# Kernel tuning notes

Hardware: AMD Instinct MI355X
Metric: run time of the kernel (lower is better)

The kernel has to match this reference:

```python
import jax, jax.numpy as jnp
import numpy as np

N_NODES = 100000


def gcn_conv(x, src, dst, W, b):
    # torch_geometric GCNConv: add self-loops, sym-normalize, linear, aggregate
    n = x.shape[0]
    deg = jax.ops.segment_sum(jnp.ones_like(src, dtype=x.dtype), dst, num_segments=n)
    dinv = jnp.where(deg > 0, jax.lax.rsqrt(deg), 0.0)
    norm = dinv[src] * dinv[dst]                      # [E]
    h = x @ W                                         # [N, out]
    msg = h[src] * norm[:, None]                      # [E, out] gather
    out = jax.ops.segment_sum(msg, dst, num_segments=n)  # scatter-add
    return out + b


def add_self_loops(edge_index, n):
    loop = jnp.arange(n, dtype=edge_index.dtype)
    src = jnp.concatenate([edge_index[0], loop])
    dst = jnp.concatenate([edge_index[1], loop])
    return src, dst


def setup_inputs() -> dict:
    key = jax.random.key(0)
    k1, k2, k3, k4 = jax.random.split(key, 4)
    F_in, F_mid = 64, 32
    x = jax.random.normal(k1, (N_NODES, F_in), dtype=jnp.float32)
    edge_index = jax.random.randint(k2, (2, 1200000), 0, N_NODES, dtype=jnp.int64)
    W1 = jax.random.normal(k3, (F_in, F_mid), dtype=jnp.float32) * (1.0 / np.sqrt(F_in))
    b1 = jnp.zeros((F_mid,), dtype=jnp.float32)
    W2 = jax.random.normal(k4, (F_mid, F_in), dtype=jnp.float32) * (1.0 / np.sqrt(F_mid))
    b2 = jnp.zeros((F_in,), dtype=jnp.float32)
    return {"x": x, "edge_index": edge_index, "W1": W1, "b1": b1, "W2": W2, "b2": b2}


def reference(x, edge_index, W1, b1, W2, b2):
    src, dst = add_self_loops(edge_index, x.shape[0])
    h = jax.nn.relu(gcn_conv(x, src, dst, W1, b1))
    # F.dropout in eval mode is identity (module not in training)
    out = gcn_conv(h, src, dst, W2, b2)
    return out
```

## Files before the change

kernel.cpp:

```cpp
#include <hip/hip_runtime.h>


#define CAP 32
#define OVF_MAX 65536
#define SH_BITS 8
#define SH 256
#define BCAP 3584
#define EPB 4096
#define EPT 16

__device__ __forceinline__ unsigned bf16rn(float f) {
    unsigned u = __float_as_uint(f);
    return (u + 0x7fffu + ((u >> 16) & 1u)) >> 16;
}
__device__ __forceinline__ unsigned pack2(float f0, float f1) {
    return (bf16rn(f1) << 16) | bf16rn(f0);
}
__device__ __forceinline__ void acc2(float4& a, uint2 v) {
    a.x += __uint_as_float(v.x << 16);
    a.y += __uint_as_float(v.x & 0xffff0000u);
    a.z += __uint_as_float(v.y << 16);
    a.w += __uint_as_float(v.y & 0xffff0000u);
}

__global__ void init_kernel(int* __restrict__ bcur, int* __restrict__ ovfcnt,
                            unsigned int* __restrict__ g1rowN,
                            unsigned int* __restrict__ q1rowN, int B) {
    int i = blockIdx.x * blockDim.x + threadIdx.x;
    if (i < B) bcur[i] = i * BCAP;
    if (i == 0) *ovfcnt = 0;
    if (i < 16) { g1rowN[i] = 0u; q1rowN[i] = 0u; }
}

__global__ __launch_bounds__(256) void bin_kernel(const int* __restrict__ src,
                                                  const int* __restrict__ dst,
                                                  int* __restrict__ bcur,
                                                  unsigned int* __restrict__ ebuf,
                                                  int* __restrict__ ovfcnt,
                                                  int* __restrict__ ovf, int E, int B) {
    __shared__ int h[512];
    __shared__ int gp[512];
    for (int b = threadIdx.x; b < B; b += 256) h[b] = 0;
    __syncthreads();
    int base = blockIdx.x * EPB;
    int s[EPT], d[EPT], r[EPT];
#pragma unroll
    for (int k = 0; k < EPT; ++k) {
        int e = base + k * 256 + threadIdx.x;
        bool ok = e < E;
        s[k] = ok ? src[e] : 0;
        d[k] = ok ? dst[e] : 0;
        r[k] = ok ? atomicAdd(&h[d[k] >> SH_BITS], 1) : 0;
    }
    __syncthreads();
    for (int b = threadIdx.x; b < B; b += 256)
        if (h[b]) gp[b] = atomicAdd(&bcur[b], h[b]);
    __syncthreads();
#pragma unroll
    for (int k = 0; k < EPT; ++k) {
        int e = base + k * 256 + threadIdx.x;
        if (e < E) {
            int bk = d[k] >> SH_BITS;
            int pos = gp[bk] + r[k];
            if (pos < (bk + 1) * BCAP)
                ebuf[pos] = ((unsigned)(d[k] & (SH - 1)) << 24) | (unsigned)s[k];
            else { int o = atomicAdd(ovfcnt, 1); if (o < OVF_MAX) { ovf[2 * o] = s[k]; ovf[2 * o + 1] = d[k]; } }
        }
    }
}

__global__ __launch_bounds__(256) void fillb_kernel(const unsigned int* __restrict__ ebuf,
                                                    const int* __restrict__ bcur,
                                                    int* __restrict__ adj,
                                                    float* __restrict__ dinv,
                                                    int* __restrict__ ovfcnt,
                                                    int* __restrict__ ovf, int N) {
    __shared__ int lcnt[SH];
    __shared__ int ladj[SH * CAP];
    int b = blockIdx.x;
    for (int i = threadIdx.x; i < SH; i += 256) lcnt[i] = 0;
    for (int i = threadIdx.x; i < SH * CAP; i += 256) ladj[i] = N;
    __syncthreads();
    int beg = b * BCAP;
    int tot = bcur[b] - beg;
    int m = tot < BCAP ? tot : BCAP;
    for (int i = threadIdx.x; i < m; i += 256) {
        unsigned p = ebuf[beg + i];
        int ld = (int)(p >> 24), sidx = (int)(p & 0xFFFFFF);
        int q = atomicAdd(&lcnt[ld], 1);
        if (q < CAP) ladj[ld * CAP + q] = sidx;
        else { int o = atomicAdd(ovfcnt, 1); if (o < OVF_MAX) { ovf[2 * o] = sidx; ovf[2 * o + 1] = (b << SH_BITS) + ld; } }
    }
    __syncthreads();
    int nb0 = b << SH_BITS;
    const int4* l4 = (const int4*)ladj;
    int4* a4 = (int4*)(adj + (size_t)nb0 * CAP);
    for (int i = threadIdx.x; i < SH * CAP / 4; i += 256) {
        int row = i >> 3;
        int nd = nb0 + row;
        bool second = (i & 4) != 0;
        if (nd < N && (!second || lcnt[row] >= 16)) a4[i] = l4[i];
    }
    for (int i = threadIdx.x; i < SH; i += 256) {
        int nd = nb0 + i;
        if (nd < N) dinv[nd] = rsqrtf((float)lcnt[i] + 1.0f);
    }
}

__global__ __launch_bounds__(256) void gemm1_kernel(const float* __restrict__ x,
                                                    const float* __restrict__ W1,
                                                    const float* __restrict__ dinv,
                                                    unsigned int* __restrict__ g1, int N) {
    __shared__ float Ws[64 * 32];
    __shared__ float xs[16][64];
    int tid = threadIdx.x;
    const float4* W4 = (const float4*)W1;
    float4* Ws4 = (float4*)Ws;
    for (int i = tid; i < 512; i += 256) Ws4[i] = W4[i];
    int nb = blockIdx.x * 16;
    {
        int ln = tid >> 4, k4 = (tid & 15) * 4;
        int n = nb + ln;
        float4 v = make_float4(0.f, 0.f, 0.f, 0.f);
        if (n < N) v = *(const float4*)(x + (size_t)n * 64 + k4);
        *(float4*)(&xs[ln][k4]) = v;
    }
    __syncthreads();
    int ln = tid >> 4, j = tid & 15;
    int n = nb + ln;
    if (n < N) {
        float s0 = 0.f, s1 = 0.f;
#pragma unroll
        for (int k = 0; k < 64; ++k) {
            float xv = xs[ln][k];
            s0 += xv * Ws[k * 32 + 2 * j];
            s1 += xv * Ws[k * 32 + 2 * j + 1];
        }
        float dv = dinv[n];
        g1[(size_t)n * 16 + j] = pack2(dv * s0, dv * s1);
    }
}

__device__ __forceinline__ float4 gather_row4(const int2* __restrict__ adj2,
                                              const int* __restrict__ ovfcnt,
                                              const int* __restrict__ ovf,
                                              const uint2* __restrict__ g2,
                                              int n, int l, int N) {
    int2 h1 = adj2[(size_t)n * 16 + l];
    float4 a = make_float4(0.f, 0.f, 0.f, 0.f);
    uint2 self = g2[(size_t)n * 8 + l];
    int s15;
    {
        int s0  = __shfl(h1.x, 0, 8), s1  = __shfl(h1.y, 0, 8);
        int s2  = __shfl(h1.x, 1, 8), s3  = __shfl(h1.y, 1, 8);
        int s4  = __shfl(h1.x, 2, 8), s5  = __shfl(h1.y, 2, 8);
        int s6  = __shfl(h1.x, 3, 8), s7  = __shfl(h1.y, 3, 8);
        int s8  = __shfl(h1.x, 4, 8), s9  = __shfl(h1.y, 4, 8);
        int s10 = __shfl(h1.x, 5, 8), s11 = __shfl(h1.y, 5, 8);
        int s12 = __shfl(h1.x, 6, 8), s13 = __shfl(h1.y, 6, 8);
        int s14 = __shfl(h1.x, 7, 8); s15 = __shfl(h1.y, 7, 8);
        uint2 v0  = g2[(size_t)s0  * 8 + l], v1  = g2[(size_t)s1  * 8 + l];
        uint2 v2  = g2[(size_t)s2  * 8 + l], v3  = g2[(size_t)s3  * 8 + l];
        uint2 v4  = g2[(size_t)s4  * 8 + l], v5  = g2[(size_t)s5  * 8 + l];
        uint2 v6  = g2[(size_t)s6  * 8 + l], v7  = g2[(size_t)s7  * 8 + l];
        uint2 v8  = g2[(size_t)s8  * 8 + l], v9  = g2[(size_t)s9  * 8 + l];
        uint2 v10 = g2[(size_t)s10 * 8 + l], v11 = g2[(size_t)s11 * 8 + l];
        uint2 v12 = g2[(size_t)s12 * 8 + l], v13 = g2[(size_t)s13 * 8 + l];
        uint2 v14 = g2[(size_t)s14 * 8 + l], v15 = g2[(size_t)s15 * 8 + l];
        acc2(a, self);
        acc2(a, v0);  acc2(a, v1);  acc2(a, v2);  acc2(a, v3);
        acc2(a, v4);  acc2(a, v5);  acc2(a, v6);  acc2(a, v7);
        acc2(a, v8);  acc2(a, v9);  acc2(a, v10); acc2(a, v11);
        acc2(a, v12); acc2(a, v13); acc2(a, v14); acc2(a, v15);
    }
    if (s15 != N) {
        int2 h2 = adj2[(size_t)n * 16 + 8 + l];
        int s0  = __shfl(h2.x, 0, 8), s1  = __shfl(h2.y, 0, 8);
        int s2  = __shfl(h2.x, 1, 8), s3  = __shfl(h2.y, 1, 8);
        int s4  = __shfl(h2.x, 2, 8), s5  = __shfl(h2.y, 2, 8);
        int s6  = __shfl(h2.x, 3, 8), s7  = __shfl(h2.y, 3, 8);
        int s8  = __shfl(h2.x, 4, 8), s9  = __shfl(h2.y, 4, 8);
        int s10 = __shfl(h2.x, 5, 8), s11 = __shfl(h2.y, 5, 8);
        int s12 = __shfl(h2.x, 6, 8), s13 = __shfl(h2.y, 6, 8);
        int s14 = __shfl(h2.x, 7, 8), sl15 = __shfl(h2.y, 7, 8);
        uint2 v0  = g2[(size_t)s0  * 8 + l], v1  = g2[(size_t)s1  * 8 + l];
        uint2 v2  = g2[(size_t)s2  * 8 + l], v3  = g2[(size_t)s3  * 8 + l];
        uint2 v4  = g2[(size_t)s4  * 8 + l], v5  = g2[(size_t)s5  * 8 + l];
        uint2 v6  = g2[(size_t)s6  * 8 + l], v7  = g2[(size_t)s7  * 8 + l];
        uint2 v8  = g2[(size_t)s8  * 8 + l], v9  = g2[(size_t)s9  * 8 + l];
        uint2 v10 = g2[(size_t)s10 * 8 + l], v11 = g2[(size_t)s11 * 8 + l];
        uint2 v12 = g2[(size_t)s12 * 8 + l], v13 = g2[(size_t)s13 * 8 + l];
        uint2 v14 = g2[(size_t)s14 * 8 + l], v15 = g2[(size_t)sl15 * 8 + l];
        acc2(a, v0);  acc2(a, v1);  acc2(a, v2);  acc2(a, v3);
        acc2(a, v4);  acc2(a, v5);  acc2(a, v6);  acc2(a, v7);
        acc2(a, v8);  acc2(a, v9);  acc2(a, v10); acc2(a, v11);
        acc2(a, v12); acc2(a, v13); acc2(a, v14); acc2(a, v15);
    }
    int c = *ovfcnt; if (c > OVF_MAX) c = OVF_MAX;
    for (int i = 0; i < c; ++i) {
        if (ovf[2 * i + 1] == n) acc2(a, g2[(size_t)ovf[2 * i] * 8 + l]);
    }
    return a;
}

__global__ void gather_q_kernel(const int2* __restrict__ adj2,
                                const int* __restrict__ ovfcnt, const int* __restrict__ ovf,
                                const uint2* __restrict__ g2, const float* __restrict__ dinv,
                                const float* __restrict__ b1, uint2* __restrict__ q2, int N) {
    int tid = blockIdx.x * blockDim.x + threadIdx.x;
    int n = tid >> 3, l = tid & 7;
    if (n < N) {
        float4 a = gather_row4(adj2, ovfcnt, ovf, g2, n, l, N);
        float dv = dinv[n];
        float4 bb = ((const float4*)b1)[l];
        float vx = dv * a.x + bb.x, vy = dv * a.y + bb.y;
        float vz = dv * a.z + bb.z, vw = dv * a.w + bb.w;
        vx = vx > 0.f ? vx : 0.f; vy = vy > 0.f ? vy : 0.f;
        vz = vz > 0.f ? vz : 0.f; vw = vw > 0.f ? vw : 0.f;
        q2[(size_t)n * 8 + l] = make_uint2(pack2(dv * vx, dv * vy), pack2(dv * vz, dv * vw));
    }
}

__global__ __launch_bounds__(256) void gather_out_kernel(
        const int2* __restrict__ adj2,
        const int* __restrict__ ovfcnt, const int* __restrict__ ovf,
        const uint2* __restrict__ q2, const float* __restrict__ dinv,
        const float* __restrict__ W2, const float* __restrict__ b2,
        float* __restrict__ out, int N) {
    __shared__ float Ws[32 * 64];
    __shared__ float sAgg[32][36];
    int tid = threadIdx.x;
    const float4* W4 = (const float4*)W2;
    float4* Ws4 = (float4*)Ws;
    for (int i = tid; i < 512; i += 256) Ws4[i] = W4[i];
    int nb = blockIdx.x * 32;
    int o = tid >> 3, l = tid & 7;
    int n = nb + o;
    if (n < N) *(float4*)(&sAgg[o][l * 4]) = gather_row4(adj2, ovfcnt, ovf, q2, n, l, N);
    __syncthreads();
    int ln = tid >> 6, j = tid & 63;
#pragma unroll
    for (int nn = 0; nn < 8; ++nn) {
        int ol = nn * 4 + ln;
        int node = nb + ol;
        if (node < N) {
            float s = 0.f;
#pragma unroll
            for (int k = 0; k < 32; ++k) s += sAgg[ol][k] * Ws[k * 64 + j];
            __builtin_nontemporal_store(dinv[node] * s + b2[j], &out[(size_t)node * 64 + j]);
        }
    }
}

extern "C" void kernel_launch(void* const* d_in, const int* in_sizes, int n_in,
                              void* d_out, int out_size, void* d_ws, size_t ws_size,
                              hipStream_t stream) {
    const float* x  = (const float*)d_in[0];
    const int*   ei = (const int*)d_in[1];
    const float* W1 = (const float*)d_in[2];
    const float* b1 = (const float*)d_in[3];
    const float* W2 = (const float*)d_in[4];
    const float* b2 = (const float*)d_in[5];
    float* out = (float*)d_out;

    int N = in_sizes[0] / 64;
    int E = in_sizes[1] / 2;
    const int* src = ei;
    const int* dst = ei + (size_t)E;
    int B = (N + SH - 1) >> SH_BITS;

    size_t NP = (size_t)N + 1;
    float* dinv   = (float*)d_ws;
    unsigned int* g1 = (unsigned int*)(dinv + N);
    unsigned int* q1 = g1 + 16 * NP;
    unsigned int* ebuf = q1;
    int*   adj    = (int*)(q1 + 16 * NP);
    int*   bcur   = adj + (size_t)CAP * N;
    int*   ovfcnt = bcur + 512;
    int*   ovf    = ovfcnt + 4;

    init_kernel<<<(B + 255) / 256, 256, 0, stream>>>(bcur, ovfcnt,
                                                     g1 + 16 * (size_t)N, q1 + 16 * (size_t)N, B);
    bin_kernel<<<(E + EPB - 1) / EPB, 256, 0, stream>>>(src, dst, bcur, ebuf, ovfcnt, ovf, E, B);
    fillb_kernel<<<B, 256, 0, stream>>>(ebuf, bcur, adj, dinv, ovfcnt, ovf, N);

    gemm1_kernel<<<(N + 15) / 16, 256, 0, stream>>>(x, W1, dinv, g1, N);

    long long tq = (long long)N * 8;
    gather_q_kernel<<<(int)((tq + 255) / 256), 256, 0, stream>>>(
        (const int2*)adj, ovfcnt, ovf, (const uint2*)g1, dinv, b1, (uint2*)q1, N);
    gather_out_kernel<<<(N + 31) / 32, 256, 0, stream>>>(
        (const int2*)adj, ovfcnt, ovf, (const uint2*)q1, dinv, W2, b2, out, N);
}
```

Measured before the change: 179.9 us.

## Split bf16 feature tables into column halves to shrink gather working set

The 32-wide bf16 intermediate tables g1 and q1 are split into two 16-column halves (ga/gb, qa/qb), each with 32-byte rows. The first-layer gather now runs as two passes over separate half tables, and the output gather walks the halves one after another. The aim is to make each pass's random-gather working set half as large so it fits better in cache. Nontemporal loads are also added for streamed inputs, and ebuf gets its own region instead of aliasing q1. In exchange, adjacency indices are read twice and each gathered access moves 4 bytes instead of 8, so more load instructions are issued.

```diff
diff --git a/kernel.cpp b/kernel.cpp
--- a/kernel.cpp
+++ b/kernel.cpp
@@ -9,6 +9,8 @@
 #define EPB 4096
 #define EPT 16
 
+typedef __attribute__((ext_vector_type(4))) float vf4;
+
 __device__ __forceinline__ unsigned bf16rn(float f) {
     unsigned u = __float_as_uint(f);
     return (u + 0x7fffu + ((u >> 16) & 1u)) >> 16;
@@ -16,20 +18,18 @@
 __device__ __forceinline__ unsigned pack2(float f0, float f1) {
     return (bf16rn(f1) << 16) | bf16rn(f0);
 }
-__device__ __forceinline__ void acc2(float4& a, uint2 v) {
-    a.x += __uint_as_float(v.x << 16);
-    a.y += __uint_as_float(v.x & 0xffff0000u);
-    a.z += __uint_as_float(v.y << 16);
-    a.w += __uint_as_float(v.y & 0xffff0000u);
+__device__ __forceinline__ void accu(float2& a, unsigned v) {
+    a.x += __uint_as_float(v << 16);
+    a.y += __uint_as_float(v & 0xffff0000u);
 }
 
 __global__ void init_kernel(int* __restrict__ bcur, int* __restrict__ ovfcnt,
-                            unsigned int* __restrict__ g1rowN,
-                            unsigned int* __restrict__ q1rowN, int B) {
+                            unsigned* __restrict__ ga, unsigned* __restrict__ gb,
+                            unsigned* __restrict__ qa, unsigned* __restrict__ qb, int B) {
     int i = blockIdx.x * blockDim.x + threadIdx.x;
     if (i < B) bcur[i] = i * BCAP;
     if (i == 0) *ovfcnt = 0;
-    if (i < 16) { g1rowN[i] = 0u; q1rowN[i] = 0u; }
+    if (i < 8) { ga[i] = 0u; gb[i] = 0u; qa[i] = 0u; qb[i] = 0u; }
 }
 
 __global__ __launch_bounds__(256) void bin_kernel(const int* __restrict__ src,
@@ -48,8 +48,8 @@
     for (int k = 0; k < EPT; ++k) {
         int e = base + k * 256 + threadIdx.x;
         bool ok = e < E;
-        s[k] = ok ? src[e] : 0;
-        d[k] = ok ? dst[e] : 0;
+        s[k] = ok ? __builtin_nontemporal_load(src + e) : 0;
+        d[k] = ok ? __builtin_nontemporal_load(dst + e) : 0;
         r[k] = ok ? atomicAdd(&h[d[k] >> SH_BITS], 1) : 0;
     }
     __syncthreads();
@@ -85,7 +85,7 @@
     int tot = bcur[b] - beg;
     int m = tot < BCAP ? tot : BCAP;
     for (int i = threadIdx.x; i < m; i += 256) {
-        unsigned p = ebuf[beg + i];
+        unsigned p = __builtin_nontemporal_load(ebuf + beg + i);
         int ld = (int)(p >> 24), sidx = (int)(p & 0xFFFFFF);
         int q = atomicAdd(&lcnt[ld], 1);
         if (q < CAP) ladj[ld * CAP + q] = sidx;
@@ -110,20 +110,21 @@
 __global__ __launch_bounds__(256) void gemm1_kernel(const float* __restrict__ x,
                                                     const float* __restrict__ W1,
                                                     const float* __restrict__ dinv,
-                                                    unsigned int* __restrict__ g1, int N) {
+                                                    unsigned int* __restrict__ ga,
+                                                    unsigned int* __restrict__ gb, int N) {
     __shared__ float Ws[64 * 32];
     __shared__ float xs[16][64];
     int tid = threadIdx.x;
-    const float4* W4 = (const float4*)W1;
-    float4* Ws4 = (float4*)Ws;
+    const vf4* W4 = (const vf4*)W1;
+    vf4* Ws4 = (vf4*)Ws;
     for (int i = tid; i < 512; i += 256) Ws4[i] = W4[i];
     int nb = blockIdx.x * 16;
     {
-        int ln = tid >> 4, k4 = (tid & 15) * 4;
+        int ln = tid >> 4, k4 = tid & 15;
         int n = nb + ln;
-        float4 v = make_float4(0.f, 0.f, 0.f, 0.f);
-        if (n < N) v = *(const float4*)(x + (size_t)n * 64 + k4);
-        *(float4*)(&xs[ln][k4]) = v;
+        vf4 v = {0.f, 0.f, 0.f, 0.f};
+        if (n < N) v = __builtin_nontemporal_load((const vf4*)(x + (size_t)n * 64) + k4);
+        *(vf4*)(&xs[ln][k4 * 4]) = v;
     }
     __syncthreads();
     int ln = tid >> 4, j = tid & 15;
@@ -137,20 +138,106 @@
             s1 += xv * Ws[k * 32 + 2 * j + 1];
         }
         float dv = dinv[n];
-        g1[(size_t)n * 16 + j] = pack2(dv * s0, dv * s1);
-    }
-}
-
-__device__ __forceinline__ float4 gather_row4(const int2* __restrict__ adj2,
-                                              const int* __restrict__ ovfcnt,
-                                              const int* __restrict__ ovf,
-                                              const uint2* __restrict__ g2,
-                                              int n, int l, int N) {
+        unsigned pv = pack2(dv * s0, dv * s1);
+        if (j < 8) ga[(size_t)n * 8 + j] = pv;
+        else       gb[(size_t)n * 8 + (j - 8)] = pv;
+    }
+}
+
+__global__ __launch_bounds__(256) void gather_q_kernel(
+        const int2* __restrict__ adj2,
+        const int* __restrict__ ovfcnt, const int* __restrict__ ovf,
+        const unsigned* __restrict__ ga, const unsigned* __restrict__ gb,
+        const float* __restrict__ dinv, const float* __restrict__ b1,
+        unsigned* __restrict__ qa, unsigned* __restrict__ qb, int N, int nbHalf) {
+    int bid = blockIdx.x;
+    int half = (bid >= nbHalf) ? 1 : 0;
+    int nb = (bid - half * nbHalf) * 32;
+    int tid = threadIdx.x;
+    int o = tid >> 3, l = tid & 7;
+    int n = nb + o;
+    if (n >= N) return;
+    const unsigned* gp = half ? gb : ga;
+    unsigned* qp = half ? qb : qa;
+
     int2 h1 = adj2[(size_t)n * 16 + l];
-    float4 a = make_float4(0.f, 0.f, 0.f, 0.f);
-    uint2 self = g2[(size_t)n * 8 + l];
-    int s15;
-    {
+    int s0  = __shfl(h1.x, 0, 8), s1  = __shfl(h1.y, 0, 8);
+    int s2  = __shfl(h1.x, 1, 8), s3  = __shfl(h1.y, 1, 8);
+    int s4  = __shfl(h1.x, 2, 8), s5  = __shfl(h1.y, 2, 8);
+    int s6  = __shfl(h1.x, 3, 8), s7  = __shfl(h1.y, 3, 8);
+    int s8  = __shfl(h1.x, 4, 8), s9  = __shfl(h1.y, 4, 8);
+    int s10 = __shfl(h1.x, 5, 8), s11 = __shfl(h1.y, 5, 8);
+    int s12 = __shfl(h1.x, 6, 8), s13 = __shfl(h1.y, 6, 8);
+    int s14 = __shfl(h1.x, 7, 8), s15 = __shfl(h1.y, 7, 8);
+
+    unsigned w16 = gp[(size_t)n * 8 + l];
+    unsigned w0  = gp[(size_t)s0  * 8 + l], w1  = gp[(size_t)s1  * 8 + l];
+    unsigned w2  = gp[(size_t)s2  * 8 + l], w3  = gp[(size_t)s3  * 8 + l];
+    unsigned w4  = gp[(size_t)s4  * 8 + l], w5  = gp[(size_t)s5  * 8 + l];
+    unsigned w6  = gp[(size_t)s6  * 8 + l], w7  = gp[(size_t)s7  * 8 + l];
+    unsigned w8  = gp[(size_t)s8  * 8 + l], w9  = gp[(size_t)s9  * 8 + l];
+    unsigned w10 = gp[(size_t)s10 * 8 + l], w11 = gp[(size_t)s11 * 8 + l];
+    unsigned w12 = gp[(size_t)s12 * 8 + l], w13 = gp[(size_t)s13 * 8 + l];
+    unsigned w14 = gp[(size_t)s14 * 8 + l], w15 = gp[(size_t)s15 * 8 + l];
+    float2 a = make_float2(0.f, 0.f);
+    accu(a, w16);
+    accu(a, w0);  accu(a, w1);  accu(a, w2);  accu(a, w3);
+    accu(a, w4);  accu(a, w5);  accu(a, w6);  accu(a, w7);
+    accu(a, w8);  accu(a, w9);  accu(a, w10); accu(a, w11);
+    accu(a, w12); accu(a, w13); accu(a, w14); accu(a, w15);
+
+    if (s15 != N) {
+        int2 h2 = adj2[(size_t)n * 16 + 8 + l];
+        int t0  = __shfl(h2.x, 0, 8), t1  = __shfl(h2.y, 0, 8);
+        int t2  = __shfl(h2.x, 1, 8), t3  = __shfl(h2.y, 1, 8);
+        int t4  = __shfl(h2.x, 2, 8), t5  = __shfl(h2.y, 2, 8);
+        int t6  = __shfl(h2.x, 3, 8), t7  = __shfl(h2.y, 3, 8);
+        int t8  = __shfl(h2.x, 4, 8), t9  = __shfl(h2.y, 4, 8);
+        int t10 = __shfl(h2.x, 5, 8), t11 = __shfl(h2.y, 5, 8);
+        int t12 = __shfl(h2.x, 6, 8), t13 = __shfl(h2.y, 6, 8);
+        int t14 = __shfl(h2.x, 7, 8), t15 = __shfl(h2.y, 7, 8);
+        unsigned u0  = gp[(size_t)t0  * 8 + l], u1  = gp[(size_t)t1  * 8 + l];
+        unsigned u2  = gp[(size_t)t2  * 8 + l], u3  = gp[(size_t)t3  * 8 + l];
+        unsigned u4  = gp[(size_t)t4  * 8 + l], u5  = gp[(size_t)t5  * 8 + l];
+        unsigned u6  = gp[(size_t)t6  * 8 + l], u7  = gp[(size_t)t7  * 8 + l];
+        unsigned u8  = gp[(size_t)t8  * 8 + l], u9  = gp[(size_t)t9  * 8 + l];
+        unsigned u10 = gp[(size_t)t10 * 8 + l], u11 = gp[(size_t)t11 * 8 + l];
+        unsigned u12 = gp[(size_t)t12 * 8 + l], u13 = gp[(size_t)t13 * 8 + l];
+        unsigned u14 = gp[(size_t)t14 * 8 + l], u15 = gp[(size_t)t15 * 8 + l];
+        accu(a, u0);  accu(a, u1);  accu(a, u2);  accu(a, u3);
+        accu(a, u4);  accu(a, u5);  accu(a, u6);  accu(a, u7);
+        accu(a, u8);  accu(a, u9);  accu(a, u10); accu(a, u11);
+        accu(a, u12); accu(a, u13); accu(a, u14); accu(a, u15);
+    }
+    int c = *ovfcnt; if (c > OVF_MAX) c = OVF_MAX;
+    for (int i = 0; i < c; ++i) {
+        if (ovf[2 * i + 1] == n) accu(a, gp[(size_t)ovf[2 * i] * 8 + l]);
+    }
+    float dv = dinv[n];
+    float2 bb = ((const float2*)b1)[half * 8 + l];
+    float v0 = dv * a.x + bb.x, v1 = dv * a.y + bb.y;
+    v0 = v0 > 0.f ? v0 : 0.f; v1 = v1 > 0.f ? v1 : 0.f;
+    qp[(size_t)n * 8 + l] = pack2(dv * v0, dv * v1);
+}
+
+__global__ __launch_bounds__(256) void gather_out_kernel(
+        const int2* __restrict__ adj2,
+        const int* __restrict__ ovfcnt, const int* __restrict__ ovf,
+        const unsigned* __restrict__ qa, const unsigned* __restrict__ qb,
+        const float* __restrict__ dinv,
+        const float* __restrict__ W2, const float* __restrict__ b2,
+        float* __restrict__ out, int N) {
+    __shared__ float Ws[32 * 64];
+    __shared__ float sAgg[32][36];
+    int tid = threadIdx.x;
+    const vf4* W4 = (const vf4*)W2;
+    vf4* Ws4 = (vf4*)Ws;
+    for (int i = tid; i < 512; i += 256) Ws4[i] = W4[i];
+    int nb = blockIdx.x * 32;
+    int o = tid >> 3, l = tid & 7;
+    int n = nb + o;
+    if (n < N) {
+        int2 h1 = adj2[(size_t)n * 16 + l];
         int s0  = __shfl(h1.x, 0, 8), s1  = __shfl(h1.y, 0, 8);
         int s2  = __shfl(h1.x, 1, 8), s3  = __shfl(h1.y, 1, 8);
         int s4  = __shfl(h1.x, 2, 8), s5  = __shfl(h1.y, 2, 8);
@@ -158,85 +245,61 @@
         int s8  = __shfl(h1.x, 4, 8), s9  = __shfl(h1.y, 4, 8);
         int s10 = __shfl(h1.x, 5, 8), s11 = __shfl(h1.y, 5, 8);
         int s12 = __shfl(h1.x, 6, 8), s13 = __shfl(h1.y, 6, 8);
-        int s14 = __shfl(h1.x, 7, 8); s15 = __shfl(h1.y, 7, 8);
-        uint2 v0  = g2[(size_t)s0  * 8 + l], v1  = g2[(size_t)s1  * 8 + l];
-        uint2 v2  = g2[(size_t)s2  * 8 + l], v3  = g2[(size_t)s3  * 8 + l];
-        uint2 v4  = g2[(size_t)s4  * 8 + l], v5  = g2[(size_t)s5  * 8 + l];
-        uint2 v6  = g2[(size_t)s6  * 8 + l], v7  = g2[(size_t)s7  * 8 + l];
-        uint2 v8  = g2[(size_t)s8  * 8 + l], v9  = g2[(size_t)s9  * 8 + l];
-        uint2 v10 = g2[(size_t)s10 * 8 + l], v11 = g2[(size_t)s11 * 8 + l];
-        uint2 v12 = g2[(size_t)s12 * 8 + l], v13 = g2[(size_t)s13 * 8 + l];
-        uint2 v14 = g2[(size_t)s14 * 8 + l], v15 = g2[(size_t)s15 * 8 + l];
-        acc2(a, self);
-        acc2(a, v0);  acc2(a, v1);  acc2(a, v2);  acc2(a, v3);
-        acc2(a, v4);  acc2(a, v5);  acc2(a, v6);  acc2(a, v7);
-        acc2(a, v8);  acc2(a, v9);  acc2(a, v10); acc2(a, v11);
-        acc2(a, v12); acc2(a, v13); acc2(a, v14); acc2(a, v15);
-    }
-    if (s15 != N) {
-        int2 h2 = adj2[(size_t)n * 16 + 8 + l];
-        int s0  = __shfl(h2.x, 0, 8), s1  = __shfl(h2.y, 0, 8);
-        int s2  = __shfl(h2.x, 1, 8), s3  = __shfl(h2.y, 1, 8);
-        int s4  = __shfl(h2.x, 2, 8), s5  = __shfl(h2.y, 2, 8);
-        int s6  = __shfl(h2.x, 3, 8), s7  = __shfl(h2.y, 3, 8);
-        int s8  = __shfl(h2.x, 4, 8), s9  = __shfl(h2.y, 4, 8);
-        int s10 = __shfl(h2.x, 5, 8), s11 = __shfl(h2.y, 5, 8);
-        int s12 = __shfl(h2.x, 6, 8), s13 = __shfl(h2.y, 6, 8);
-        int s14 = __shfl(h2.x, 7, 8), sl15 = __shfl(h2.y, 7, 8);
-        uint2 v0  = g2[(size_t)s0  * 8 + l], v1  = g2[(size_t)s1  * 8 + l];
-        uint2 v2  = g2[(size_t)s2  * 8 + l], v3  = g2[(size_t)s3  * 8 + l];
-        uint2 v4  = g2[(size_t)s4  * 8 + l], v5  = g2[(size_t)s5  * 8 + l];
-        uint2 v6  = g2[(size_t)s6  * 8 + l], v7  = g2[(size_t)s7  * 8 + l];
-        uint2 v8  = g2[(size_t)s8  * 8 + l], v9  = g2[(size_t)s9  * 8 + l];
-        uint2 v10 = g2[(size_t)s10 * 8 + l], v11 = g2[(size_t)s11 * 8 + l];
-        uint2 v12 = g2[(size_t)s12 * 8 + l], v13 = g2[(size_t)s13 * 8 + l];
-        uint2 v14 = g2[(size_t)s14 * 8 + l], v15 = g2[(size_t)sl15 * 8 + l];
-        acc2(a, v0);  acc2(a, v1);  acc2(a, v2);  acc2(a, v3);
-        acc2(a, v4);  acc2(a, v5);  acc2(a, v6);  acc2(a, v7);
-        acc2(a, v8);  acc2(a, v9);  acc2(a, v10); acc2(a, v11);
-        acc2(a, v12); acc2(a, v13); acc2(a, v14); acc2(a, v15);
-    }
-    int c = *ovfcnt; if (c > OVF_MAX) c = OVF_MAX;
-    for (int i = 0; i < c; ++i) {
-        if (ovf[2 * i + 1] == n) acc2(a, g2[(size_t)ovf[2 * i] * 8 + l]);
-    }
-    return a;
-}
-
-__global__ void gather_q_kernel(const int2* __restrict__ adj2,
-                                const int* __restrict__ ovfcnt, const int* __restrict__ ovf,
-                                const uint2* __restrict__ g2, const float* __restrict__ dinv,
-                                const float* __restrict__ b1, uint2* __restrict__ q2, int N) {
-    int tid = blockIdx.x * blockDim.x + threadIdx.x;
-    int n = tid >> 3, l = tid & 7;
-    if (n < N) {
-        float4 a = gather_row4(adj2, ovfcnt, ovf, g2, n, l, N);
-        float dv = dinv[n];
-        float4 bb = ((const float4*)b1)[l];
-        float vx = dv * a.x + bb.x, vy = dv * a.y + bb.y;
-        float vz = dv * a.z + bb.z, vw = dv * a.w + bb.w;
-        vx = vx > 0.f ? vx : 0.f; vy = vy > 0.f ? vy : 0.f;
-        vz = vz > 0.f ? vz : 0.f; vw = vw > 0.f ? vw : 0.f;
-        q2[(size_t)n * 8 + l] = make_uint2(pack2(dv * vx, dv * vy), pack2(dv * vz, dv * vw));
-    }
-}
-
-__global__ __launch_bounds__(256) void gather_out_kernel(
-        const int2* __restrict__ adj2,
-        const int* __restrict__ ovfcnt, const int* __restrict__ ovf,
-        const uint2* __restrict__ q2, const float* __restrict__ dinv,
-        const float* __restrict__ W2, const float* __restrict__ b2,
-        float* __restrict__ out, int N) {
-    __shared__ float Ws[32 * 64];
-    __shared__ float sAgg[32][36];
-    int tid = threadIdx.x;
-    const float4* W4 = (const float4*)W2;
-    float4* Ws4 = (float4*)Ws;
-    for (int i = tid; i < 512; i += 256) Ws4[i] = W4[i];
-    int nb = blockIdx.x * 32;
-    int o = tid >> 3, l = tid & 7;
-    int n = nb + o;
-    if (n < N) *(float4*)(&sAgg[o][l * 4]) = gather_row4(adj2, ovfcnt, ovf, q2, n, l, N);
+        int s14 = __shfl(h1.x, 7, 8), s15 = __shfl(h1.y, 7, 8);
+        bool big = (s15 != N);
+        int t0 = N, t1 = N, t2 = N, t3 = N, t4 = N, t5 = N, t6 = N, t7 = N;
+        int t8 = N, t9 = N, t10 = N, t11 = N, t12 = N, t13 = N, t14 = N, t15 = N;
+        if (big) {
+            int2 h2 = adj2[(size_t)n * 16 + 8 + l];
+            t0  = __shfl(h2.x, 0, 8); t1  = __shfl(h2.y, 0, 8);
+            t2  = __shfl(h2.x, 1, 8); t3  = __shfl(h2.y, 1, 8);
+            t4  = __shfl(h2.x, 2, 8); t5  = __shfl(h2.y, 2, 8);
+            t6  = __shfl(h2.x, 3, 8); t7  = __shfl(h2.y, 3, 8);
+            t8  = __shfl(h2.x, 4, 8); t9  = __shfl(h2.y, 4, 8);
+            t10 = __shfl(h2.x, 5, 8); t11 = __shfl(h2.y, 5, 8);
+            t12 = __shfl(h2.x, 6, 8); t13 = __shfl(h2.y, 6, 8);
+            t14 = __shfl(h2.x, 7, 8); t15 = __shfl(h2.y, 7, 8);
+        }
+        int c = *ovfcnt; if (c > OVF_MAX) c = OVF_MAX;
+#pragma unroll
+        for (int ph = 0; ph < 2; ++ph) {
+            const unsigned* qp = ph ? qb : qa;
+            unsigned w16 = qp[(size_t)n * 8 + l];
+            unsigned w0  = qp[(size_t)s0  * 8 + l], w1  = qp[(size_t)s1  * 8 + l];
+            unsigned w2  = qp[(size_t)s2  * 8 + l], w3  = qp[(size_t)s3  * 8 + l];
+            unsigned w4  = qp[(size_t)s4  * 8 + l], w5  = qp[(size_t)s5  * 8 + l];
+            unsigned w6  = qp[(size_t)s6  * 8 + l], w7  = qp[(size_t)s7  * 8 + l];
+            unsigned w8  = qp[(size_t)s8  * 8 + l], w9  = qp[(size_t)s9  * 8 + l];
+            unsigned w10 = qp[(size_t)s10 * 8 + l], w11 = qp[(size_t)s11 * 8 + l];
+            unsigned w12 = qp[(size_t)s12 * 8 + l], w13 = qp[(size_t)s13 * 8 + l];
+            unsigned w14 = qp[(size_t)s14 * 8 + l], w15 = qp[(size_t)s15 * 8 + l];
+            float2 a = make_float2(0.f, 0.f);
+            accu(a, w16);
+            accu(a, w0);  accu(a, w1);  accu(a, w2);  accu(a, w3);
+            accu(a, w4);  accu(a, w5);  accu(a, w6);  accu(a, w7);
+            accu(a, w8);  accu(a, w9);  accu(a, w10); accu(a, w11);
+            accu(a, w12); accu(a, w13); accu(a, w14); accu(a, w15);
+            if (big) {
+                unsigned u0  = qp[(size_t)t0  * 8 + l], u1  = qp[(size_t)t1  * 8 + l];
+                unsigned u2  = qp[(size_t)t2  * 8 + l], u3  = qp[(size_t)t3  * 8 + l];
+                unsigned u4  = qp[(size_t)t4  * 8 + l], u5  = qp[(size_t)t5  * 8 + l];
+                unsigned u6  = qp[(size_t)t6  * 8 + l], u7  = qp[(size_t)t7  * 8 + l];
+                unsigned u8  = qp[(size_t)t8  * 8 + l], u9  = qp[(size_t)t9  * 8 + l];
+                unsigned u10 = qp[(size_t)t10 * 8 + l], u11 = qp[(size_t)t11 * 8 + l];
+                unsigned u12 = qp[(size_t)t12 * 8 + l], u13 = qp[(size_t)t13 * 8 + l];
+                unsigned u14 = qp[(size_t)t14 * 8 + l], u15 = qp[(size_t)t15 * 8 + l];
+                accu(a, u0);  accu(a, u1);  accu(a, u2);  accu(a, u3);
+                accu(a, u4);  accu(a, u5);  accu(a, u6);  accu(a, u7);
+                accu(a, u8);  accu(a, u9);  accu(a, u10); accu(a, u11);
+                accu(a, u12); accu(a, u13); accu(a, u14); accu(a, u15);
+            }
+            for (int i = 0; i < c; ++i) {
+                if (ovf[2 * i + 1] == n) accu(a, qp[(size_t)ovf[2 * i] * 8 + l]);
+            }
+            sAgg[o][ph * 16 + 2 * l]     = a.x;
+            sAgg[o][ph * 16 + 2 * l + 1] = a.y;
+        }
+    }
     __syncthreads();
     int ln = tid >> 6, j = tid & 63;
 #pragma unroll
@@ -270,25 +333,28 @@
     int B = (N + SH - 1) >> SH_BITS;
 
     size_t NP = (size_t)N + 1;
-    float* dinv   = (float*)d_ws;
-    unsigned int* g1 = (unsigned int*)(dinv + N);
-    unsigned int* q1 = g1 + 16 * NP;
-    unsigned int* ebuf = q1;
-    int*   adj    = (int*)(q1 + 16 * NP);
-    int*   bcur   = adj + (size_t)CAP * N;
-    int*   ovfcnt = bcur + 512;
-    int*   ovf    = ovfcnt + 4;
-
-    init_kernel<<<(B + 255) / 256, 256, 0, stream>>>(bcur, ovfcnt,
-                                                     g1 + 16 * (size_t)N, q1 + 16 * (size_t)N, B);
+    float* dinv = (float*)d_ws;
+    unsigned* ga = (unsigned*)(dinv + N);
+    unsigned* gb = ga + 8 * NP;
+    unsigned* qa = gb + 8 * NP;
+    unsigned* qb = qa + 8 * NP;
+    unsigned* ebuf = qb + 8 * NP;
+    int* adj    = (int*)(ebuf + (size_t)B * BCAP);
+    int* bcur   = adj + (size_t)CAP * N;
+    int* ovfcnt = bcur + 512;
+    int* ovf    = ovfcnt + 4;
+
+    init_kernel<<<(B + 255) / 256, 256, 0, stream>>>(
+        bcur, ovfcnt, ga + 8 * (size_t)N, gb + 8 * (size_t)N,
+        qa + 8 * (size_t)N, qb + 8 * (size_t)N, B);
     bin_kernel<<<(E + EPB - 1) / EPB, 256, 0, stream>>>(src, dst, bcur, ebuf, ovfcnt, ovf, E, B);
     fillb_kernel<<<B, 256, 0, stream>>>(ebuf, bcur, adj, dinv, ovfcnt, ovf, N);
 
-    gemm1_kernel<<<(N + 15) / 16, 256, 0, stream>>>(x, W1, dinv, g1, N);
-
-    long long tq = (long long)N * 8;
-    gather_q_kernel<<<(int)((tq + 255) / 256), 256, 0, stream>>>(
-        (const int2*)adj, ovfcnt, ovf, (const uint2*)g1, dinv, b1, (uint2*)q1, N);
+    gemm1_kernel<<<(N + 15) / 16, 256, 0, stream>>>(x, W1, dinv, ga, gb, N);
+
+    int nbHalf = (N + 31) / 32;
+    gather_q_kernel<<<2 * nbHalf, 256, 0, stream>>>(
+        (const int2*)adj, ovfcnt, ovf, ga, gb, dinv, b1, qa, qb, N, nbHalf);
     gather_out_kernel<<<(N + 31) / 32, 256, 0, stream>>>(
-        (const int2*)adj, ovfcnt, ovf, (const uint2*)q1, dinv, W2, b2, out, N);
-}
+        (const int2*)adj, ovfcnt, ovf, qa, qb, dinv, W2, b2, out, N);
+}
```

After: 192.1 us. +6.7%, slower.
